# Kernel tuning notes

Measured on AMD Instinct MI355X. Metric: run time of the kernel, lower is better.

Reference implementation:

```python
import jax, jax.numpy as jnp
import numpy as np

NQ, NK, E, DIM, H = 100000, 100000, 1600000, 128, 8
DH = DIM // H
LN_EPS = 1e-5


def _prelu(x, w):
    return jnp.where(x >= 0, x, w * x)


def setup_inputs() -> dict:
    key = jax.random.key(0)
    ks = jax.random.split(key, 12)
    s = 1.0 / np.sqrt(DIM)
    return {
        "query": jax.random.normal(ks[0], (NQ, DIM), jnp.float32),
        "keys": jax.random.normal(ks[1], (NK, DIM), jnp.float32),
        "values": jax.random.normal(ks[2], (NK, DIM), jnp.float32),
        "query_idx": jax.random.randint(ks[3], (E,), 0, NQ),
        "key_idx": jax.random.randint(ks[4], (E,), 0, NK),
        "Wq": jax.random.normal(ks[5], (DIM, DIM), jnp.float32) * s,
        "bq": jnp.zeros((DIM,), jnp.float32),
        "Wk": jax.random.normal(ks[6], (DIM, DIM), jnp.float32) * s,
        "bk": jnp.zeros((DIM,), jnp.float32),
        "Wv": jax.random.normal(ks[7], (DIM, DIM), jnp.float32) * s,
        "bv": jnp.zeros((DIM,), jnp.float32),
        "Wp": jax.random.normal(ks[8], (DIM, DIM), jnp.float32) * s,
        "bp": jnp.zeros((DIM,), jnp.float32),
        "a": jax.random.normal(ks[9], (1, H, DH), jnp.float32) * 0.1,
        "prelu_w": jnp.full((1,), 0.25, jnp.float32),
        "ln_g": jnp.ones((DIM,), jnp.float32),
        "ln_b": jnp.zeros((DIM,), jnp.float32),
    }


def reference(query, keys, values, query_idx, key_idx, Wq, bq, Wk, bk, Wv, bv,
              Wp, bp, a, prelu_w, ln_g, ln_b):
    nq = query.shape[0]
    # node-level projections, then per-edge gather (project-then-gather branch)
    Qp = query @ Wq.T + bq                      # [NQ, DIM]
    Kp = keys @ Wk.T + bk                       # [NK, DIM]
    # per-edge additive attention score: [E, H, 1]
    e = (a * _prelu(Qp[query_idx] + Kp[key_idx], prelu_w).reshape(-1, H, DH)).sum(-1, keepdims=True)
    # segment max (index_reduce amax, initialized at global min, detached)
    min_attn = jnp.min(e)
    max_q = jnp.full((nq, H, 1), min_attn, e.dtype).at[query_idx].max(e)
    max_q = jax.lax.stop_gradient(max_q)
    # segment softmax
    exp_e = jnp.exp(e - max_q[query_idx])       # [E, H, 1]
    denom = jnp.zeros((nq, H, 1), e.dtype).at[query_idx].add(exp_e)
    denom = jnp.where(denom == 0, jnp.asarray(1.0, e.dtype), denom)
    # weighted value aggregation (value_idx == key_idx here)
    Vv = (values @ Wv.T + bv)[key_idx].reshape(-1, H, DH)  # [E, H, DH]
    msg = jnp.zeros((nq, H, DH), e.dtype).at[query_idx].add(exp_e * Vv)
    # output projection + residual + LayerNorm (dropout is identity at eval)
    x = query + ((msg / denom).reshape(nq, DIM) @ Wp.T + bp)
    mu = x.mean(-1, keepdims=True)
    var = ((x - mu) ** 2).mean(-1, keepdims=True)
    return (x - mu) / jnp.sqrt(var + LN_EPS) * ln_g + ln_b
```

## Files before the change

kernel.cpp:

```cpp
#include <hip/hip_runtime.h>
#include <hip/hip_bf16.h>

#define DIMN 128
#define LN_EPS 1e-5f

typedef __bf16 bf16x8 __attribute__((ext_vector_type(8)));
typedef float f32x4 __attribute__((ext_vector_type(4)));

__device__ __forceinline__ float bf_even(uint32_t u) {
    union { uint32_t u; float f; } c; c.u = u << 16; return c.f;
}
__device__ __forceinline__ float bf_odd(uint32_t u) {
    union { uint32_t u; float f; } c; c.u = u & 0xffff0000u; return c.f;
}

__device__ __forceinline__ float head_reduce(float e) {
    int x = __float_as_int(e);
    e += __int_as_float(__builtin_amdgcn_ds_swizzle(x, 0x041F));
    x = __float_as_int(e);
    e += __int_as_float(__builtin_amdgcn_ds_swizzle(x, 0x081F));
    x = __float_as_int(e);
    e += __int_as_float(__builtin_amdgcn_ds_swizzle(x, 0x101F));
    return e;
}

__global__ __launch_bounds__(256) void k_prep(
        const float* __restrict__ Wq, const float* __restrict__ Wk,
        const float* __restrict__ Wv, const float* __restrict__ Wp,
        __bf16* __restrict__ wsplit, const int* __restrict__ qidx,
        int* __restrict__ counts, int* __restrict__ rank, int E) {
    int bi = blockIdx.x;
    if (bi < 256) {
        int w = bi >> 6;
        const float* W = (w == 0) ? Wq : (w == 1) ? Wk : (w == 2) ? Wv : Wp;
        __bf16* hi = wsplit + (size_t)w * 32768;
        __bf16* lo = hi + 16384;
        int i = (bi & 63) * 256 + threadIdx.x;
        float x = W[i];
        __bf16 h = (__bf16)x;
        hi[i] = h;
        lo[i] = (__bf16)(x - (float)h);
    } else {
        int i = (bi - 256) * 256 + threadIdx.x;
        if (i < E) rank[i] = atomicAdd(&counts[qidx[i]], 1);
    }
}

__global__ __launch_bounds__(256, 1) void k_proj2(
        const float* __restrict__ query, const float* __restrict__ keys,
        const float* __restrict__ values, const __bf16* __restrict__ wsplit,
        const float* __restrict__ bq, const float* __restrict__ bk,
        const float* __restrict__ bv, float* __restrict__ Qp,
        __bf16* __restrict__ KV, int NQ_, int NK_,
        const int* __restrict__ counts, int* __restrict__ offs,
        int* __restrict__ bsum, int nb) {
    __shared__ int s[256];
    if ((int)blockIdx.x < nb) {
        int t = threadIdx.x;
        int i = blockIdx.x * 256 + t;
        int v = (i < NQ_) ? counts[i] : 0;
        s[t] = v;
        __syncthreads();
        for (int o = 1; o < 256; o <<= 1) {
            int x = (t >= o) ? s[t - o] : 0;
            __syncthreads();
            s[t] += x;
            __syncthreads();
        }
        if (i < NQ_) offs[i] = s[t] - v;
        if (t == 255) bsum[blockIdx.x] = s[t];
    }

    int lane = threadIdx.x & 63;
    int wid  = threadIdx.x >> 6;
    int r = lane & 15, g = lane >> 4;
    int rowoff = (wid >> 1) * 16;
    int chalf  = wid & 1;

    int ntq = (NQ_ + 31) >> 5;
    int ntk = (NK_ + 31) >> 5;
    int total = ntq + 2 * ntk;

    int mode = -1;
    bf16x8 Bf[4][4][2];
    float  bias_n[4];

    for (int t = blockIdx.x; t < total; t += gridDim.x) {
        int m, tt;
        if (t < ntq)            { m = 0; tt = t; }
        else if (t < ntq + ntk) { m = 1; tt = t - ntq; }
        else                    { m = 2; tt = t - ntq - ntk; }

        if (m != mode) {
            mode = m;
            const __bf16* wh = wsplit + (size_t)m * 32768;
            const __bf16* wl = wh + 16384;
            const float* bias = (m == 0) ? bq : (m == 1) ? bk : bv;
#pragma unroll
            for (int c = 0; c < 4; ++c) {
                int n = (chalf * 4 + c) * 16 + r;
#pragma unroll
                for (int ks = 0; ks < 4; ++ks) {
                    Bf[c][ks][0] = *(const bf16x8*)(wh + n * DIMN + ks * 32 + g * 8);
                    Bf[c][ks][1] = *(const bf16x8*)(wl + n * DIMN + ks * 32 + g * 8);
                }
                bias_n[c] = bias[n];
            }
        }

        const float* X = (m == 0) ? query : (m == 1) ? keys : values;
        int M = (m == 0) ? NQ_ : NK_;
        int rb = tt * 32 + rowoff;
        int arow = rb + r; if (arow >= M) arow = M - 1;
        const float* xrow = X + (size_t)arow * DIMN;

        bf16x8 Ah[4], Al[4];
#pragma unroll
        for (int ks = 0; ks < 4; ++ks) {
            const float* px = xrow + ks * 32 + g * 8;
            f32x4 v0 = *(const f32x4*)(px);
            f32x4 v1 = *(const f32x4*)(px + 4);
#pragma unroll
            for (int i = 0; i < 4; ++i) {
                __bf16 h0 = (__bf16)v0[i];
                __bf16 h1 = (__bf16)v1[i];
                Ah[ks][i]     = h0;
                Ah[ks][i + 4] = h1;
                Al[ks][i]     = (__bf16)(v0[i] - (float)h0);
                Al[ks][i + 4] = (__bf16)(v1[i] - (float)h1);
            }
        }

        f32x4 acc[4];
#pragma unroll
        for (int c = 0; c < 4; ++c) {
            acc[c] = (f32x4){0.f, 0.f, 0.f, 0.f};
#pragma unroll
            for (int ks = 0; ks < 4; ++ks) {
                acc[c] = __builtin_amdgcn_mfma_f32_16x16x32_bf16(Ah[ks], Bf[c][ks][0], acc[c], 0, 0, 0);
                acc[c] = __builtin_amdgcn_mfma_f32_16x16x32_bf16(Ah[ks], Bf[c][ks][1], acc[c], 0, 0, 0);
                acc[c] = __builtin_amdgcn_mfma_f32_16x16x32_bf16(Al[ks], Bf[c][ks][0], acc[c], 0, 0, 0);
            }
        }

        if (m == 0) {
#pragma unroll
            for (int c = 0; c < 4; ++c) {
                int n = (chalf * 4 + c) * 16 + r;
#pragma unroll
                for (int i = 0; i < 4; ++i) {
                    int row = rb + g * 4 + i;
                    if (row < M) Qp[(size_t)row * DIMN + n] = acc[c][i] + bias_n[c];
                }
            }
        } else {
            int vofs = (m == 2) ? 128 : 0;
#pragma unroll
            for (int c = 0; c < 4; ++c) {
                int n = (chalf * 4 + c) * 16 + r;
#pragma unroll
                for (int i = 0; i < 4; ++i) {
                    int row = rb + g * 4 + i;
                    if (row < M) KV[(size_t)row * 256 + vofs + n] = (__bf16)(acc[c][i] + bias_n[c]);
                }
            }
        }
    }
}

__global__ __launch_bounds__(1024) void k_scan2(int* __restrict__ bsum, int nb) {
    __shared__ int s[1024];
    int t = threadIdx.x;
    int v = (t < nb) ? bsum[t] : 0;
    s[t] = v;
    __syncthreads();
    for (int o = 1; o < 1024; o <<= 1) {
        int x = (t >= o) ? s[t - o] : 0;
        __syncthreads();
        s[t] += x;
        __syncthreads();
    }
    if (t < nb) bsum[t] = s[t];
}

__global__ void k_scatter(const int* __restrict__ qidx, const int* __restrict__ kidx,
                          const int* __restrict__ offs, const int* __restrict__ bsum,
                          const int* __restrict__ rank, int* __restrict__ skey, int E) {
    int i = blockIdx.x * 256 + threadIdx.x;
    if (i < E) {
        int q = qidx[i];
        int base = offs[q] + ((q >= 256) ? bsum[(q >> 8) - 1] : 0);
        skey[base + rank[i]] = kidx[i];
    }
}

__global__ __launch_bounds__(256) void k_attn(
        const float* __restrict__ Qp, const __bf16* __restrict__ KV,
        const int* __restrict__ offs, const int* __restrict__ bsum,
        const int* __restrict__ skey, const float* __restrict__ a,
        const float* __restrict__ prelu_w, float* __restrict__ msg,
        int NQ_, int E_) {
    int lane = threadIdx.x & 63;
    int q = blockIdx.x * 4 + (threadIdx.x >> 6);
    if (q >= NQ_) return;
    int d = lane * 2;
    float2 av = *(const float2*)(a + d);
    float a0 = av.x, a1 = av.y;
    float pw = prelu_w[0];
    float2 qv = *(const float2*)(Qp + (size_t)q * DIMN + d);
    float q0 = qv.x, q1 = qv.y;
    int beg = offs[q] + ((q >= 256) ? bsum[(q >> 8) - 1] : 0);
    int qn = q + 1;
    int end = (qn == NQ_) ? E_ : offs[qn] + ((qn >= 256) ? bsum[(qn >> 8) - 1] : 0);

    float den = 0.f, acc0 = 0.f, acc1 = 0.f;
    int j = beg;
    for (; j + 3 < end; j += 4) {
        int k0 = skey[j], k1 = skey[j + 1], k2 = skey[j + 2], k3 = skey[j + 3];
        const uint32_t* r0 = (const uint32_t*)(KV + ((size_t)k0 << 8));
        const uint32_t* r1 = (const uint32_t*)(KV + ((size_t)k1 << 8));
        const uint32_t* r2 = (const uint32_t*)(KV + ((size_t)k2 << 8));
        const uint32_t* r3 = (const uint32_t*)(KV + ((size_t)k3 << 8));
        uint32_t ku0 = r0[lane], ku1 = r1[lane], ku2 = r2[lane], ku3 = r3[lane];
        uint32_t vu0 = r0[64 + lane], vu1 = r1[64 + lane], vu2 = r2[64 + lane], vu3 = r3[64 + lane];

        float e0, e1, e2, e3;
        {
            float s0 = q0 + bf_even(ku0), s1 = q1 + bf_odd(ku0);
            s0 = s0 >= 0.f ? s0 : pw * s0;  s1 = s1 >= 0.f ? s1 : pw * s1;
            e0 = a0 * s0 + a1 * s1;
        }
        {
            float s0 = q0 + bf_even(ku1), s1 = q1 + bf_odd(ku1);
            s0 = s0 >= 0.f ? s0 : pw * s0;  s1 = s1 >= 0.f ? s1 : pw * s1;
            e1 = a0 * s0 + a1 * s1;
        }
        {
            float s0 = q0 + bf_even(ku2), s1 = q1 + bf_odd(ku2);
            s0 = s0 >= 0.f ? s0 : pw * s0;  s1 = s1 >= 0.f ? s1 : pw * s1;
            e2 = a0 * s0 + a1 * s1;
        }
        {
            float s0 = q0 + bf_even(ku3), s1 = q1 + bf_odd(ku3);
            s0 = s0 >= 0.f ? s0 : pw * s0;  s1 = s1 >= 0.f ? s1 : pw * s1;
            e3 = a0 * s0 + a1 * s1;
        }
        e0 = head_reduce(e0);
        e1 = head_reduce(e1);
        e2 = head_reduce(e2);
        e3 = head_reduce(e3);
        float w0 = __expf(e0), w1 = __expf(e1), w2 = __expf(e2), w3 = __expf(e3);
        den  += (w0 + w1) + (w2 + w3);
        acc0 += w0 * bf_even(vu0) + w1 * bf_even(vu1) + w2 * bf_even(vu2) + w3 * bf_even(vu3);
        acc1 += w0 * bf_odd(vu0)  + w1 * bf_odd(vu1)  + w2 * bf_odd(vu2)  + w3 * bf_odd(vu3);
    }
    for (; j < end; ++j) {
        int k = skey[j];
        const uint32_t* r_ = (const uint32_t*)(KV + ((size_t)k << 8));
        uint32_t ku = r_[lane], vu = r_[64 + lane];
        float s0 = q0 + bf_even(ku), s1 = q1 + bf_odd(ku);
        s0 = s0 >= 0.f ? s0 : pw * s0;  s1 = s1 >= 0.f ? s1 : pw * s1;
        float e = a0 * s0 + a1 * s1;
        e = head_reduce(e);
        float w = __expf(e);
        den += w;
        acc0 += w * bf_even(vu);
        acc1 += w * bf_odd(vu);
    }
    float inv = den > 0.f ? 1.f / den : 0.f;
    float2 o; o.x = acc0 * inv; o.y = acc1 * inv;
    *(float2*)(msg + (size_t)q * DIMN + d) = o;
}

__global__ __launch_bounds__(256) void k_final(
        const float* __restrict__ msg, const __bf16* __restrict__ wh,
        const __bf16* __restrict__ wl, const float* __restrict__ bp,
        const float* __restrict__ query, const float* __restrict__ lng,
        const float* __restrict__ lnb, float* __restrict__ out, int M) {
    int lane = threadIdx.x & 63;
    int wid  = threadIdx.x >> 6;
    int r = lane & 15, g = lane >> 4;
    int rb = blockIdx.x * 64 + wid * 16;

    int arow = rb + r; if (arow >= M) arow = M - 1;
    const float* xrow = msg + (size_t)arow * DIMN;
    bf16x8 Ah[4], Al[4];
#pragma unroll
    for (int ks = 0; ks < 4; ++ks) {
        const float* px = xrow + ks * 32 + g * 8;
#pragma unroll
        for (int i = 0; i < 8; ++i) {
            float v = px[i];
            __bf16 h = (__bf16)v;
            Ah[ks][i] = h;
            Al[ks][i] = (__bf16)(v - (float)h);
        }
    }
    float xv[8][4];
#pragma unroll
    for (int ct = 0; ct < 8; ++ct) {
        f32x4 acc = {0.f, 0.f, 0.f, 0.f};
        int n = ct * 16 + r;
        const __bf16* bh = wh + n * DIMN + g * 8;
        const __bf16* bl = wl + n * DIMN + g * 8;
#pragma unroll
        for (int ks = 0; ks < 4; ++ks) {
            bf16x8 Bh = *(const bf16x8*)(bh + ks * 32);
            bf16x8 Bl = *(const bf16x8*)(bl + ks * 32);
            acc = __builtin_amdgcn_mfma_f32_16x16x32_bf16(Ah[ks], Bh, acc, 0, 0, 0);
            acc = __builtin_amdgcn_mfma_f32_16x16x32_bf16(Ah[ks], Bl, acc, 0, 0, 0);
            acc = __builtin_amdgcn_mfma_f32_16x16x32_bf16(Al[ks], Bh, acc, 0, 0, 0);
        }
        float bn = bp[n];
#pragma unroll
        for (int i = 0; i < 4; ++i) {
            int row = rb + g * 4 + i;
            int rc = row < M ? row : M - 1;
            xv[ct][i] = acc[i] + bn + query[(size_t)rc * DIMN + n];
        }
    }
#pragma unroll
    for (int i = 0; i < 4; ++i) {
        float s = 0.f, ss = 0.f;
#pragma unroll
        for (int ct = 0; ct < 8; ++ct) { s += xv[ct][i]; ss += xv[ct][i] * xv[ct][i]; }
        s += __shfl_xor(s, 1, 64);  ss += __shfl_xor(ss, 1, 64);
        s += __shfl_xor(s, 2, 64);  ss += __shfl_xor(ss, 2, 64);
        s += __shfl_xor(s, 4, 64);  ss += __shfl_xor(ss, 4, 64);
        s += __shfl_xor(s, 8, 64);  ss += __shfl_xor(ss, 8, 64);
        float mean = s * (1.f / DIMN);
        float var  = ss * (1.f / DIMN) - mean * mean;
        float rstd = rsqrtf(var + LN_EPS);
        int row = rb + g * 4 + i;
#pragma unroll
        for (int ct = 0; ct < 8; ++ct) {
            int n = ct * 16 + r;
            if (row < M)
                out[(size_t)row * DIMN + n] = (xv[ct][i] - mean) * rstd * lng[n] + lnb[n];
        }
    }
}

extern "C" void kernel_launch(void* const* d_in, const int* in_sizes, int n_in,
                              void* d_out, int out_size, void* d_ws, size_t ws_size,
                              hipStream_t stream) {
    const float* query = (const float*)d_in[0];
    const float* keys  = (const float*)d_in[1];
    const float* values= (const float*)d_in[2];
    const int*   qidx  = (const int*)d_in[3];
    const int*   kidx  = (const int*)d_in[4];
    const float* Wq    = (const float*)d_in[5];
    const float* bq    = (const float*)d_in[6];
    const float* Wk    = (const float*)d_in[7];
    const float* bk    = (const float*)d_in[8];
    const float* Wv    = (const float*)d_in[9];
    const float* bv    = (const float*)d_in[10];
    const float* Wp    = (const float*)d_in[11];
    const float* bp    = (const float*)d_in[12];
    const float* a     = (const float*)d_in[13];
    const float* pw    = (const float*)d_in[14];
    const float* lng   = (const float*)d_in[15];
    const float* lnb   = (const float*)d_in[16];

    int NQ_ = in_sizes[0] / DIMN;
    int NK_ = in_sizes[1] / DIMN;
    int E_  = in_sizes[3];

    char* p = (char*)d_ws;
    __bf16* wsplit = (__bf16*)p;
    size_t off = (size_t)4 * 32768 * sizeof(__bf16);
    float*  Qp = (float*)(p + off);  off += (size_t)NQ_ * DIMN * 4;
    __bf16* KV = (__bf16*)(p + off); off += (size_t)NK_ * 256 * 2;
    int* counts = (int*)(p + off); off += (((size_t)NQ_ * 4) + 127) / 128 * 128;
    int* offs   = (int*)(p + off); off += (((size_t)NQ_ * 4) + 127) / 128 * 128;
    int* bsum   = (int*)(p + off); off += 1024 * 4;
    int* rank   = (int*)(p + off); off += (size_t)E_ * 4;
    int* skey   = (int*)(p + off); off += (size_t)E_ * 4;
    float* msg  = Qp;

    hipMemsetAsync(counts, 0, (size_t)NQ_ * 4, stream);

    int ge = (E_ + 255) / 256;
    int gm = (NQ_ + 63) / 64;
    int nb = (NQ_ + 255) / 256;

    k_prep<<<256 + ge, 256, 0, stream>>>(Wq, Wk, Wv, Wp, wsplit, qidx, counts, rank, E_);

    k_proj2<<<2048, 256, 0, stream>>>(query, keys, values, wsplit, bq, bk, bv,
                                      Qp, KV, NQ_, NK_, counts, offs, bsum, nb);

    k_scan2<<<1, 1024, 0, stream>>>(bsum, nb);

    k_scatter<<<ge, 256, 0, stream>>>(qidx, kidx, offs, bsum, rank, skey, E_);

    k_attn<<<(NQ_ + 3) / 4, 256, 0, stream>>>(Qp, KV, offs, bsum, skey, a, pw, msg, NQ_, E_);

    k_final<<<gm, 256, 0, stream>>>(msg, wsplit + 3 * 32768, wsplit + 3 * 32768 + 16384,
                                    bp, query, lng, lnb, (float*)d_out, NQ_);
}
```

Baseline: 435.7 us.

## Stage projection weights in LDS, drop split-precision for K/V, chunk tiles per block

The projection kernel now stages the bf16 hi/lo weight matrices in padded shared memory instead of holding them in registers, and assigns each block a contiguous chunk of 5 tiles rather than grid-striding over a fixed 2048-block grid. For the K and V projections it drops the lo-part MFMAs and keeps only a single bf16 product, because those outputs are stored in bf16 anyway. This cuts MFMA work and register pressure, which allows two blocks per CU. The final projection kernel also stages its weights in LDS and uses vectorized loads for its input rows. The cost is extra LDS traffic, barriers at mode switches, and slightly lower precision for K/V.

New measurement: 363.6 us. 1.2x faster.

```diff
diff --git a/kernel.cpp b/kernel.cpp
--- a/kernel.cpp
+++ b/kernel.cpp
@@ -3,6 +3,7 @@
 
 #define DIMN 128
 #define LN_EPS 1e-5f
+#define WPAD 136
 
 typedef __bf16 bf16x8 __attribute__((ext_vector_type(8)));
 typedef float f32x4 __attribute__((ext_vector_type(4)));
@@ -46,15 +47,18 @@
     }
 }
 
-__global__ __launch_bounds__(256, 1) void k_proj2(
+__global__ __launch_bounds__(256, 2) void k_proj3(
         const float* __restrict__ query, const float* __restrict__ keys,
         const float* __restrict__ values, const __bf16* __restrict__ wsplit,
         const float* __restrict__ bq, const float* __restrict__ bk,
         const float* __restrict__ bv, float* __restrict__ Qp,
         __bf16* __restrict__ KV, int NQ_, int NK_,
         const int* __restrict__ counts, int* __restrict__ offs,
-        int* __restrict__ bsum, int nb) {
+        int* __restrict__ bsum, int nb, int chunk) {
     __shared__ int s[256];
+    __shared__ __align__(16) __bf16 WH[128 * WPAD];
+    __shared__ __align__(16) __bf16 WL[128 * WPAD];
+
     if ((int)blockIdx.x < nb) {
         int t = threadIdx.x;
         int i = blockIdx.x * 256 + t;
@@ -81,31 +85,33 @@
     int ntk = (NK_ + 31) >> 5;
     int total = ntq + 2 * ntk;
 
-    int mode = -1;
-    bf16x8 Bf[4][4][2];
-    float  bias_n[4];
-
-    for (int t = blockIdx.x; t < total; t += gridDim.x) {
+    int t0 = blockIdx.x * chunk;
+    int t1 = t0 + chunk; if (t1 > total) t1 = total;
+    int staged = -1;
+    float bias_n[4];
+
+    for (int t = t0; t < t1; ++t) {
         int m, tt;
         if (t < ntq)            { m = 0; tt = t; }
         else if (t < ntq + ntk) { m = 1; tt = t - ntq; }
         else                    { m = 2; tt = t - ntq - ntk; }
 
-        if (m != mode) {
-            mode = m;
-            const __bf16* wh = wsplit + (size_t)m * 32768;
-            const __bf16* wl = wh + 16384;
+        if (m != staged) {
+            if (staged != -1) __syncthreads();
+            const uint4* srcH = (const uint4*)(wsplit + (size_t)m * 32768);
+            const uint4* srcL = (const uint4*)(wsplit + (size_t)m * 32768 + 16384);
+#pragma unroll
+            for (int it = 0; it < 8; ++it) {
+                int cid = threadIdx.x + it * 256;
+                int n = cid >> 4, c16 = cid & 15;
+                *(uint4*)((char*)WH + n * (WPAD * 2) + c16 * 16) = srcH[cid];
+                *(uint4*)((char*)WL + n * (WPAD * 2) + c16 * 16) = srcL[cid];
+            }
+            __syncthreads();
+            staged = m;
             const float* bias = (m == 0) ? bq : (m == 1) ? bk : bv;
 #pragma unroll
-            for (int c = 0; c < 4; ++c) {
-                int n = (chalf * 4 + c) * 16 + r;
-#pragma unroll
-                for (int ks = 0; ks < 4; ++ks) {
-                    Bf[c][ks][0] = *(const bf16x8*)(wh + n * DIMN + ks * 32 + g * 8);
-                    Bf[c][ks][1] = *(const bf16x8*)(wl + n * DIMN + ks * 32 + g * 8);
-                }
-                bias_n[c] = bias[n];
-            }
+            for (int c = 0; c < 4; ++c) bias_n[c] = bias[(chalf * 4 + c) * 16 + r];
         }
 
         const float* X = (m == 0) ? query : (m == 1) ? keys : values;
@@ -126,8 +132,10 @@
                 __bf16 h1 = (__bf16)v1[i];
                 Ah[ks][i]     = h0;
                 Ah[ks][i + 4] = h1;
-                Al[ks][i]     = (__bf16)(v0[i] - (float)h0);
-                Al[ks][i + 4] = (__bf16)(v1[i] - (float)h1);
+                if (m == 0) {
+                    Al[ks][i]     = (__bf16)(v0[i] - (float)h0);
+                    Al[ks][i + 4] = (__bf16)(v1[i] - (float)h1);
+                }
             }
         }
 
@@ -135,11 +143,16 @@
 #pragma unroll
         for (int c = 0; c < 4; ++c) {
             acc[c] = (f32x4){0.f, 0.f, 0.f, 0.f};
+            int n = (chalf * 4 + c) * 16 + r;
 #pragma unroll
             for (int ks = 0; ks < 4; ++ks) {
-                acc[c] = __builtin_amdgcn_mfma_f32_16x16x32_bf16(Ah[ks], Bf[c][ks][0], acc[c], 0, 0, 0);
-                acc[c] = __builtin_amdgcn_mfma_f32_16x16x32_bf16(Ah[ks], Bf[c][ks][1], acc[c], 0, 0, 0);
-                acc[c] = __builtin_amdgcn_mfma_f32_16x16x32_bf16(Al[ks], Bf[c][ks][0], acc[c], 0, 0, 0);
+                bf16x8 Bh = *(const bf16x8*)(WH + n * WPAD + ks * 32 + g * 8);
+                acc[c] = __builtin_amdgcn_mfma_f32_16x16x32_bf16(Ah[ks], Bh, acc[c], 0, 0, 0);
+                if (m == 0) {
+                    bf16x8 Bl = *(const bf16x8*)(WL + n * WPAD + ks * 32 + g * 8);
+                    acc[c] = __builtin_amdgcn_mfma_f32_16x16x32_bf16(Ah[ks], Bl, acc[c], 0, 0, 0);
+                    acc[c] = __builtin_amdgcn_mfma_f32_16x16x32_bf16(Al[ks], Bh, acc[c], 0, 0, 0);
+                }
             }
         }
 
@@ -272,11 +285,26 @@
     *(float2*)(msg + (size_t)q * DIMN + d) = o;
 }
 
-__global__ __launch_bounds__(256) void k_final(
+__global__ __launch_bounds__(256, 2) void k_final(
         const float* __restrict__ msg, const __bf16* __restrict__ wh,
         const __bf16* __restrict__ wl, const float* __restrict__ bp,
         const float* __restrict__ query, const float* __restrict__ lng,
         const float* __restrict__ lnb, float* __restrict__ out, int M) {
+    __shared__ __align__(16) __bf16 WH[128 * WPAD];
+    __shared__ __align__(16) __bf16 WL[128 * WPAD];
+    {
+        const uint4* srcH = (const uint4*)wh;
+        const uint4* srcL = (const uint4*)wl;
+#pragma unroll
+        for (int it = 0; it < 8; ++it) {
+            int cid = threadIdx.x + it * 256;
+            int n = cid >> 4, c16 = cid & 15;
+            *(uint4*)((char*)WH + n * (WPAD * 2) + c16 * 16) = srcH[cid];
+            *(uint4*)((char*)WL + n * (WPAD * 2) + c16 * 16) = srcL[cid];
+        }
+    }
+    __syncthreads();
+
     int lane = threadIdx.x & 63;
     int wid  = threadIdx.x >> 6;
     int r = lane & 15, g = lane >> 4;
@@ -288,12 +316,16 @@
 #pragma unroll
     for (int ks = 0; ks < 4; ++ks) {
         const float* px = xrow + ks * 32 + g * 8;
-#pragma unroll
-        for (int i = 0; i < 8; ++i) {
-            float v = px[i];
-            __bf16 h = (__bf16)v;
-            Ah[ks][i] = h;
-            Al[ks][i] = (__bf16)(v - (float)h);
+        f32x4 v0 = *(const f32x4*)(px);
+        f32x4 v1 = *(const f32x4*)(px + 4);
+#pragma unroll
+        for (int i = 0; i < 4; ++i) {
+            __bf16 h0 = (__bf16)v0[i];
+            __bf16 h1 = (__bf16)v1[i];
+            Ah[ks][i]     = h0;
+            Ah[ks][i + 4] = h1;
+            Al[ks][i]     = (__bf16)(v0[i] - (float)h0);
+            Al[ks][i + 4] = (__bf16)(v1[i] - (float)h1);
         }
     }
     float xv[8][4];
@@ -301,12 +333,10 @@
     for (int ct = 0; ct < 8; ++ct) {
         f32x4 acc = {0.f, 0.f, 0.f, 0.f};
         int n = ct * 16 + r;
-        const __bf16* bh = wh + n * DIMN + g * 8;
-        const __bf16* bl = wl + n * DIMN + g * 8;
 #pragma unroll
         for (int ks = 0; ks < 4; ++ks) {
-            bf16x8 Bh = *(const bf16x8*)(bh + ks * 32);
-            bf16x8 Bl = *(const bf16x8*)(bl + ks * 32);
+            bf16x8 Bh = *(const bf16x8*)(WH + n * WPAD + ks * 32 + g * 8);
+            bf16x8 Bl = *(const bf16x8*)(WL + n * WPAD + ks * 32 + g * 8);
             acc = __builtin_amdgcn_mfma_f32_16x16x32_bf16(Ah[ks], Bh, acc, 0, 0, 0);
             acc = __builtin_amdgcn_mfma_f32_16x16x32_bf16(Ah[ks], Bl, acc, 0, 0, 0);
             acc = __builtin_amdgcn_mfma_f32_16x16x32_bf16(Al[ks], Bh, acc, 0, 0, 0);
@@ -386,8 +416,14 @@
 
     k_prep<<<256 + ge, 256, 0, stream>>>(Wq, Wk, Wv, Wp, wsplit, qidx, counts, rank, E_);
 
-    k_proj2<<<2048, 256, 0, stream>>>(query, keys, values, wsplit, bq, bk, bv,
-                                      Qp, KV, NQ_, NK_, counts, offs, bsum, nb);
+    int ntq = (NQ_ + 31) >> 5;
+    int ntk = (NK_ + 31) >> 5;
+    int total = ntq + 2 * ntk;
+    int chunk = 5;
+    int gproj = (total + chunk - 1) / chunk;
+    if (gproj < nb) gproj = nb;
+    k_proj3<<<gproj, 256, 0, stream>>>(query, keys, values, wsplit, bq, bk, bv,
+                                       Qp, KV, NQ_, NK_, counts, offs, bsum, nb, chunk);
 
     k_scan2<<<1, 1024, 0, stream>>>(bsum, nb);
 
```
